# Optimization experiments

Measured on AMD Instinct MI355X. Metric: run time of the kernel, lower is better.

The kernel has to match this reference:

```python
import jax, jax.numpy as jnp
import numpy as np

INPUT_DIM, HID, LAT, FUT = 32, 128, 64, 128
B, T = 1024, 512


def _linear(x, W, b):
    return x @ W.T + b


def _lstm_layer(xs, Wih, Whh, b):
    # xs: [T, B, D_in] -> ys: [T, B, HID], h_T: [B, HID]
    Bsz = xs.shape[1]
    h0 = jnp.zeros((Bsz, HID), xs.dtype)
    c0 = jnp.zeros((Bsz, HID), xs.dtype)

    def step(carry, xt):
        h, c = carry
        g = xt @ Wih.T + h @ Whh.T + b  # [B, 4*HID]
        i, f, gg, o = jnp.split(g, 4, axis=-1)  # torch gate order i,f,g,o
        i = jax.nn.sigmoid(i)
        f = jax.nn.sigmoid(f)
        gg = jnp.tanh(gg)
        o = jax.nn.sigmoid(o)
        c = f * c + i * gg
        h = o * jnp.tanh(c)
        return (h, c), h

    (hT, _), ys = jax.lax.scan(step, (h0, c0), xs)
    return ys, hT


def setup_inputs() -> dict:
    key = jax.random.key(0)
    ks = iter(jax.random.split(key, 40))

    def w(shape, scale=0.05):
        return (jax.random.normal(next(ks), shape, dtype=jnp.float32) * scale)

    inp = {
        "x": jax.random.normal(next(ks), (B, T, INPUT_DIM), dtype=jnp.float32),
        "eps": jax.random.normal(next(ks), (B, LAT), dtype=jnp.float32),
        "u": jax.random.uniform(next(ks), (B, LAT), dtype=jnp.float32, minval=1e-4, maxval=1 - 1e-4),
        "choice": jax.random.uniform(next(ks), (B,), dtype=jnp.float32),
        # 3-layer LSTM params (torch: W_ih [4H, D], W_hh [4H, H], fused bias)
        "Wih0": w((4 * HID, INPUT_DIM)), "Whh0": w((4 * HID, HID)), "b0": w((4 * HID,)),
        "Wih1": w((4 * HID, HID)), "Whh1": w((4 * HID, HID)), "b1": w((4 * HID,)),
        "Wih2": w((4 * HID, HID)), "Whh2": w((4 * HID, HID)), "b2": w((4 * HID,)),
        "ln_g": jnp.ones((HID,), jnp.float32), "ln_b": jnp.zeros((HID,), jnp.float32),
        "fc1_W": w((128, HID)), "fc1_b": w((128,)),
        "fc2_W": w((64, 128)), "fc2_b": w((64,)),
        "mean_W": w((LAT, 64)), "mean_b": w((LAT,)),
        "logvar_W": w((LAT, 64)), "logvar_b": w((LAT,)),
        "scale_W": w((LAT, 64)), "scale_b": w((LAT,)),
        "shape_W": w((LAT, 64)), "shape_b": w((LAT,)),
        "dec1_W": w((128, LAT)), "dec1_b": w((128,)),
        "dec2_W": w((500, 128)), "dec2_b": w((500,)),
        "out_W": w((FUT, 500)), "out_b": w((FUT,)),
        "pi_params": jnp.array([3.0, 0.01], jnp.float32),
    }
    return inp


def reference(x, eps, u, choice,
              Wih0, Whh0, b0, Wih1, Whh1, b1, Wih2, Whh2, b2,
              ln_g, ln_b, fc1_W, fc1_b, fc2_W, fc2_b,
              mean_W, mean_b, logvar_W, logvar_b,
              scale_W, scale_b, shape_W, shape_b,
              dec1_W, dec1_b, dec2_W, dec2_b, out_W, out_b, pi_params):
    # --- Encoder ---
    xs = jnp.transpose(x, (1, 0, 2))  # [T, B, D]
    ys, _ = _lstm_layer(xs, Wih0, Whh0, b0)
    ys, _ = _lstm_layer(ys, Wih1, Whh1, b1)
    _, h = _lstm_layer(ys, Wih2, Whh2, b2)  # final hidden of last layer [B, HID]
    mu = h.mean(-1, keepdims=True)
    var = jnp.mean((h - mu) ** 2, -1, keepdims=True)
    h = (h - mu) * jax.lax.rsqrt(var + 1e-5) * ln_g + ln_b
    hid = jax.nn.relu(_linear(h, fc1_W, fc1_b))
    hid = jax.nn.relu(_linear(hid, fc2_W, fc2_b))  # dropout = identity (eval)
    z_mean = _linear(hid, mean_W, mean_b)
    z_logvar = _linear(hid, logvar_W, logvar_b)
    z_scale = jnp.exp(_linear(hid, scale_W, scale_b))
    z_shape = jnp.maximum(_linear(hid, shape_W, shape_b), 1e-6)
    # --- Reparameterize (vectorized mixture select) ---
    z_gauss = z_mean + eps * jnp.exp(0.5 * z_logvar)
    z_gpd = z_scale / z_shape * ((1.0 - u) ** (-z_shape) - 1.0)
    pi = jax.nn.softmax(pi_params)
    z = jnp.where((choice < pi[0])[:, None], z_gauss, z_gpd)
    # --- Decoder ---
    d = jax.nn.relu(_linear(z, dec1_W, dec1_b))
    d = jax.nn.relu(_linear(d, dec2_W, dec2_b))  # dropout = identity (eval)
    rec = _linear(d, out_W, out_b)
    return rec, z_mean, z_logvar, z_scale, z_shape
```

## Files before the change

### kernel.cpp

```cpp
#include <hip/hip_runtime.h>
#include <math.h>

typedef __attribute__((ext_vector_type(8))) short s16x8;
typedef __attribute__((ext_vector_type(4))) float f32x4;
typedef unsigned long long ull;

constexpr float LOG2E = 1.4426950408889634f;

__device__ __forceinline__ unsigned short f2bf(float f) {
  unsigned int x = __builtin_bit_cast(unsigned int, f);
  x += 0x7fffu + ((x >> 16) & 1u);
  return (unsigned short)(x >> 16);
}
__device__ __forceinline__ float fexp2(float x) { return __builtin_amdgcn_exp2f(x); }
__device__ __forceinline__ float frcp(float x)  { return __builtin_amdgcn_rcpf(x); }

#define MFMA16(A, B, Cc) __builtin_amdgcn_mfma_f32_16x16x32_bf16((A), (B), (Cc), 0, 0, 0)

constexpr int TT = 512;
constexpr int NB = 1024;
constexpr int CH = 2;

template <int DIN, bool FIRST, bool LAST>
__device__ __forceinline__ void scan_layer(
    unsigned short* x_s,
    unsigned short* h_s,
    float* b_s,
    const float* __restrict__ xin,
    unsigned short* ys,
    const float* __restrict__ Wih, const float* __restrict__ Whh,
    const float* __restrict__ bias, float* __restrict__ hT,
    int* prog_in, int* prog_out, int bblk)
{
  constexpr int KTX = DIN / 32;
  constexpr int XM  = (DIN == 32) ? 3 : 7;
  const int tid = threadIdx.x;
  const int wv = tid >> 6, ln = tid & 63, l15 = ln & 15, lg = ln >> 4;
  const int row0 = bblk * 16;
  const int prow = tid >> 5, pcol = tid & 31;

  s16x8 bfx[4][KTX], bfh[4][4];
#pragma unroll
  for (int j = 0; j < 4; ++j) {
    const float sc = (j == 2) ? (2.0f * LOG2E) : (-LOG2E);
    const int n = j * 128 + wv * 16 + l15;
#pragma unroll
    for (int kt = 0; kt < KTX; ++kt) {
      s16x8 f;
#pragma unroll
      for (int e = 0; e < 8; ++e) f[e] = (short)f2bf(Wih[n * DIN + kt * 32 + lg * 8 + e] * sc);
      bfx[j][kt] = f;
    }
#pragma unroll
    for (int kt = 0; kt < 4; ++kt) {
      s16x8 f;
#pragma unroll
      for (int e = 0; e < 8; ++e) f[e] = (short)f2bf(Whh[n * 128 + kt * 32 + lg * 8 + e] * sc);
      bfh[j][kt] = f;
    }
  }
  b_s[tid] = bias[tid] * ((tid >> 7) == 2 ? 2.0f * LOG2E : -LOG2E);
  for (int i = tid; i < 2 * 16 * 128; i += 512) h_s[i] = 0;

  float xrf[CH];
  ull xrh[CH];
  int avail = 0;
  if (FIRST) {
#pragma unroll
    for (int s = 0; s < CH; ++s) {
      xrf[s] = xin[(size_t)(row0 + prow) * (TT * 32) + s * 32 + pcol];
      x_s[s * (16 * DIN) + prow * DIN + (pcol ^ ((prow & XM) << 3))] = f2bf(xrf[s]);
    }
  } else {
    int f;
    do { f = __hip_atomic_load(prog_in, __ATOMIC_RELAXED, __HIP_MEMORY_SCOPE_AGENT); } while (f < 1);
    avail = f * CH;
#pragma unroll
    for (int s = 0; s < CH; ++s) {
      xrh[s] = __hip_atomic_load(
          (ull*)ys + ((size_t)s * (NB * 128) + (size_t)(row0 + prow) * 128 + pcol * 4) / 4,
          __ATOMIC_RELAXED, __HIP_MEMORY_SCOPE_AGENT);
      *reinterpret_cast<ull*>(
          &x_s[s * (16 * DIN) + prow * DIN + ((pcol * 4) ^ ((prow & 7) << 3))]) = xrh[s];
    }
  }
  __syncthreads();

  float cst[4] = {0.f, 0.f, 0.f, 0.f};
  const int hcol = wv * 16 + lg * 4;

  for (int t0 = 0; t0 < TT; t0 += CH) {
    const int t1 = t0 + CH;

    if (!LAST && tid == 0 && t0 > 0)
      __hip_atomic_store(prog_out, t0 / CH, __ATOMIC_RELAXED, __HIP_MEMORY_SCOPE_AGENT);

    int f_new = 0;
    if (!FIRST && t1 < TT)
      f_new = __hip_atomic_load(prog_in, __ATOMIC_RELAXED, __HIP_MEMORY_SCOPE_AGENT);

    bool prefetched = false;
    if (t1 < TT) {
      if (FIRST) {
#pragma unroll
        for (int s = 0; s < CH; ++s)
          xrf[s] = xin[(size_t)(row0 + prow) * (TT * 32) + (t1 + s) * 32 + pcol];
        prefetched = true;
      } else if (avail >= t1 + CH) {
#pragma unroll
        for (int s = 0; s < CH; ++s)
          xrh[s] = __hip_atomic_load(
              (ull*)ys + ((size_t)(t1 + s) * (NB * 128) + (size_t)(row0 + prow) * 128 + pcol * 4) / 4,
              __ATOMIC_RELAXED, __HIP_MEMORY_SCOPE_AGENT);
        prefetched = true;
      }
    }

    f32x4 gx[CH][4];
#pragma unroll
    for (int s = 0; s < CH; ++s) {
#pragma unroll
      for (int j = 0; j < 4; ++j)
        gx[s][j] = *reinterpret_cast<const f32x4*>(&b_s[j * 128 + wv * 16 + lg * 4]);
#pragma unroll
      for (int kt = 0; kt < KTX; ++kt) {
        const s16x8 xf = *reinterpret_cast<const s16x8*>(
            &x_s[s * (16 * DIN) + l15 * DIN + ((kt * 32 + lg * 8) ^ ((l15 & XM) << 3))]);
#pragma unroll
        for (int j = 0; j < 4; ++j) gx[s][j] = MFMA16(bfx[j][kt], xf, gx[s][j]);
      }
    }

    if (t1 < TT && !prefetched) {
      int f = f_new;
      while (f * CH < t1 + CH)
        f = __hip_atomic_load(prog_in, __ATOMIC_RELAXED, __HIP_MEMORY_SCOPE_AGENT);
      f_new = f;
      avail = f * CH;
#pragma unroll
      for (int s = 0; s < CH; ++s)
        xrh[s] = __hip_atomic_load(
            (ull*)ys + ((size_t)(t1 + s) * (NB * 128) + (size_t)(row0 + prow) * 128 + pcol * 4) / 4,
            __ATOMIC_RELAXED, __HIP_MEMORY_SCOPE_AGENT);
    }

#pragma unroll
    for (int s = 0; s < CH; ++s) {
      const int t = t0 + s;
      if (s) __syncthreads();
      unsigned short* buf  = h_s + (t & 1) * (16 * 128);
      unsigned short* nbuf = h_s + ((t + 1) & 1) * (16 * 128);
      s16x8 afr[4];
#pragma unroll
      for (int kt = 0; kt < 4; ++kt)
        afr[kt] = *reinterpret_cast<const s16x8*>(
            &buf[l15 * 128 + ((kt * 32 + lg * 8) ^ ((l15 & 7) << 3))]);
      f32x4 acc[4];
#pragma unroll
      for (int j = 0; j < 4; ++j) acc[j] = gx[s][j];
#pragma unroll
      for (int kt = 0; kt < 4; ++kt)
#pragma unroll
        for (int j = 0; j < 4; ++j) acc[j] = MFMA16(bfh[j][kt], afr[kt], acc[j]);

      float hv[4];
#pragma unroll
      for (int r = 0; r < 4; ++r) {
        const float iv = frcp(1.0f + fexp2(acc[0][r]));
        const float fv = frcp(1.0f + fexp2(acc[1][r]));
        const float gv = 1.0f - 2.0f * frcp(1.0f + fexp2(acc[2][r]));
        const float ov = frcp(1.0f + fexp2(acc[3][r]));
        const float cn = fv * cst[r] + iv * gv;
        cst[r] = cn;
        const float th = 1.0f - 2.0f * frcp(1.0f + fexp2(cn * (2.0f * LOG2E)));
        hv[r] = ov * th;
      }
      unsigned int plo, phi;
      asm("v_cvt_pk_bf16_f32 %0, %1, %2" : "=v"(plo) : "v"(hv[0]), "v"(hv[1]));
      asm("v_cvt_pk_bf16_f32 %0, %1, %2" : "=v"(phi) : "v"(hv[2]), "v"(hv[3]));
      const ull hpack = (ull)plo | ((ull)phi << 32);

      *reinterpret_cast<ull*>(&nbuf[l15 * 128 + (hcol ^ ((l15 & 7) << 3))]) = hpack;

      if (!LAST) {
        __hip_atomic_store(
            (ull*)ys + ((size_t)t * (NB * 128) + (size_t)(row0 + l15) * 128 + hcol) / 4,
            hpack, __ATOMIC_RELAXED, __HIP_MEMORY_SCOPE_AGENT);
      } else if (t == TT - 1) {
        f32x4 o = {hv[0], hv[1], hv[2], hv[3]};
        *reinterpret_cast<f32x4*>(&hT[(row0 + l15) * 128 + hcol]) = o;
      }

      if (s == CH - 1 && t1 < TT) {
        if (FIRST) {
#pragma unroll
          for (int ss = 0; ss < CH; ++ss)
            x_s[ss * (16 * DIN) + prow * DIN + (pcol ^ ((prow & XM) << 3))] = f2bf(xrf[ss]);
        } else {
#pragma unroll
          for (int ss = 0; ss < CH; ++ss)
            *reinterpret_cast<ull*>(
                &x_s[ss * (16 * DIN) + prow * DIN + ((pcol * 4) ^ ((prow & 7) << 3))]) = xrh[ss];
        }
      }
    }

    if (!FIRST && t1 < TT) {
      const int a2 = f_new * CH;
      if (a2 > avail) avail = a2;
    }

    __syncthreads();
  }

  if (!LAST && tid == 0)
    __hip_atomic_store(prog_out, TT / CH, __ATOMIC_RELAXED, __HIP_MEMORY_SCOPE_AGENT);
}

__global__ __launch_bounds__(512, 2) void lstm_fused(
    const float* __restrict__ x, unsigned short* ys,
    const float* __restrict__ Wih0, const float* __restrict__ Whh0, const float* __restrict__ b0,
    const float* __restrict__ Wih1, const float* __restrict__ Whh1, const float* __restrict__ b1,
    const float* __restrict__ Wih2, const float* __restrict__ Whh2, const float* __restrict__ b2,
    float* __restrict__ hT, int* prog)
{
  __shared__ unsigned short x_s[CH * 16 * 128];
  __shared__ unsigned short h_s[2 * 16 * 128];
  __shared__ float b_s[512];
  const int lay = blockIdx.x >> 6;
  const int bblk = blockIdx.x & 63;
  if (lay == 0) {
    scan_layer<32, true, false>(x_s, h_s, b_s, x, ys, Wih0, Whh0, b0, nullptr,
                                nullptr, &prog[(0 * 64 + bblk) * 16], bblk);
  } else if (lay == 1) {
    scan_layer<128, false, false>(x_s, h_s, b_s, nullptr, ys, Wih1, Whh1, b1, nullptr,
                                  &prog[(0 * 64 + bblk) * 16], &prog[(1 * 64 + bblk) * 16], bblk);
  } else {
    scan_layer<128, false, true>(x_s, h_s, b_s, nullptr, ys, Wih2, Whh2, b2, hT,
                                 &prog[(1 * 64 + bblk) * 16], nullptr, bblk);
  }
}

__global__ void init_flags(int* prog) {
  prog[threadIdx.x] = 0;
  prog[threadIdx.x + 1024] = 0;
}

__global__ __launch_bounds__(256) void head_kernel(
    const float* __restrict__ hT, const float* __restrict__ eps,
    const float* __restrict__ u, const float* __restrict__ choice,
    const float* __restrict__ ln_g, const float* __restrict__ ln_b,
    const float* __restrict__ fc1_W, const float* __restrict__ fc1_b,
    const float* __restrict__ fc2_W, const float* __restrict__ fc2_b,
    const float* __restrict__ mean_W, const float* __restrict__ mean_b,
    const float* __restrict__ logvar_W, const float* __restrict__ logvar_b,
    const float* __restrict__ scale_W, const float* __restrict__ scale_b,
    const float* __restrict__ shape_W, const float* __restrict__ shape_b,
    const float* __restrict__ dec1_W, const float* __restrict__ dec1_b,
    const float* __restrict__ dec2_W, const float* __restrict__ dec2_b,
    const float* __restrict__ out_W, const float* __restrict__ out_b,
    const float* __restrict__ pi_params, float* __restrict__ out)
{
  __shared__ float s_hn[4][128];
  __shared__ float s_a[4][128];
  __shared__ float s_b2[4][64];
  __shared__ float s_z[4][64];
  __shared__ float s_d1[4][128];
  __shared__ float s_d2[4][512];

  const int tid = threadIdx.x;
  const int gr0 = blockIdx.x * 4;

  {
    const int wvr = tid >> 6, lnn = tid & 63;
    const float v0 = hT[(gr0 + wvr) * 128 + lnn];
    const float v1 = hT[(gr0 + wvr) * 128 + 64 + lnn];
    float s = v0 + v1, s2 = v0 * v0 + v1 * v1;
#pragma unroll
    for (int off = 32; off; off >>= 1) {
      s  += __shfl_xor(s, off, 64);
      s2 += __shfl_xor(s2, off, 64);
    }
    const float mu  = s * (1.f / 128.f);
    const float var = s2 * (1.f / 128.f) - mu * mu;
    const float rs  = rsqrtf(var + 1e-5f);
    s_hn[wvr][lnn]      = (v0 - mu) * rs * ln_g[lnn]      + ln_b[lnn];
    s_hn[wvr][lnn + 64] = (v1 - mu) * rs * ln_g[lnn + 64] + ln_b[lnn + 64];
  }
  __syncthreads();
#pragma unroll
  for (int p = 0; p < 2; ++p) {
    const int idx = tid + p * 256, row = idx >> 7, col = idx & 127;
    const float* w = fc1_W + col * 128;
    float a = fc1_b[col];
    for (int k = 0; k < 128; k += 4)
      a += s_hn[row][k] * w[k] + s_hn[row][k + 1] * w[k + 1] +
           s_hn[row][k + 2] * w[k + 2] + s_hn[row][k + 3] * w[k + 3];
    s_a[row][col] = fmaxf(a, 0.f);
  }
  __syncthreads();
  {
    const int row = tid >> 6, col = tid & 63;
    const float* w = fc2_W + col * 128;
    float a = fc2_b[col];
    for (int k = 0; k < 128; ++k) a += s_a[row][k] * w[k];
    s_b2[row][col] = fmaxf(a, 0.f);
  }
  __syncthreads();
  {
    const int row = tid >> 6, c = tid & 63;
    const int gr = gr0 + row;
    float am = mean_b[c], al = logvar_b[c], as_ = scale_b[c], ah = shape_b[c];
    for (int k = 0; k < 64; ++k) {
      const float hv = s_b2[row][k];
      am  += hv * mean_W[c * 64 + k];
      al  += hv * logvar_W[c * 64 + k];
      as_ += hv * scale_W[c * 64 + k];
      ah  += hv * shape_W[c * 64 + k];
    }
    const float zsc = fexp2(as_ * LOG2E);
    const float zsh = fmaxf(ah, 1e-6f);
    out[131072 + gr * 64 + c] = am;
    out[196608 + gr * 64 + c] = al;
    out[262144 + gr * 64 + c] = zsc;
    out[327680 + gr * 64 + c] = zsh;
    const float ev = eps[gr * 64 + c], uv = u[gr * 64 + c], cv = choice[gr];
    const float zg = am + ev * fexp2(0.72134752044448170f * al);
    const float p0 = pi_params[0], p1 = pi_params[1];
    const float pi0 = 1.f / (1.f + expf(p1 - p0));
    const float tq = -zsh * logf(1.f - uv);
    const float zp = zsc * frcp(zsh) * expm1f(tq);
    s_z[row][c] = (cv < pi0) ? zg : zp;
  }
  __syncthreads();
#pragma unroll
  for (int p = 0; p < 2; ++p) {
    const int idx = tid + p * 256, row = idx >> 7, col = idx & 127;
    const float* w = dec1_W + col * 64;
    float a = dec1_b[col];
    for (int k = 0; k < 64; ++k) a += s_z[row][k] * w[k];
    s_d1[row][col] = fmaxf(a, 0.f);
  }
  __syncthreads();
  for (int o = tid; o < 2000; o += 256) {
    const int row = o / 500, col = o % 500;
    const float* w = dec2_W + col * 128;
    float a = dec2_b[col];
    for (int k = 0; k < 128; ++k) a += s_d1[row][k] * w[k];
    s_d2[row][col] = fmaxf(a, 0.f);
  }
  __syncthreads();
#pragma unroll
  for (int p = 0; p < 2; ++p) {
    const int idx = tid + p * 256, row = idx >> 7, col = idx & 127;
    const float* w = out_W + col * 500;
    float a = out_b[col];
    for (int k = 0; k < 500; ++k) a += s_d2[row][k] * w[k];
    out[(gr0 + row) * 128 + col] = a;
  }
}

extern "C" void kernel_launch(void* const* d_in, const int* in_sizes, int n_in,
                              void* d_out, int out_size, void* d_ws, size_t ws_size,
                              hipStream_t stream) {
  const float* x      = (const float*)d_in[0];
  const float* eps    = (const float*)d_in[1];
  const float* u      = (const float*)d_in[2];
  const float* choice = (const float*)d_in[3];
  const float* Wih0 = (const float*)d_in[4],  *Whh0 = (const float*)d_in[5],  *b0 = (const float*)d_in[6];
  const float* Wih1 = (const float*)d_in[7],  *Whh1 = (const float*)d_in[8],  *b1 = (const float*)d_in[9];
  const float* Wih2 = (const float*)d_in[10], *Whh2 = (const float*)d_in[11], *b2 = (const float*)d_in[12];
  const float* ln_g = (const float*)d_in[13], *ln_b = (const float*)d_in[14];
  const float* fc1_W = (const float*)d_in[15], *fc1_b = (const float*)d_in[16];
  const float* fc2_W = (const float*)d_in[17], *fc2_b = (const float*)d_in[18];
  const float* mean_W = (const float*)d_in[19], *mean_b = (const float*)d_in[20];
  const float* logvar_W = (const float*)d_in[21], *logvar_b = (const float*)d_in[22];
  const float* scale_W = (const float*)d_in[23], *scale_b = (const float*)d_in[24];
  const float* shape_W = (const float*)d_in[25], *shape_b = (const float*)d_in[26];
  const float* dec1_W = (const float*)d_in[27], *dec1_b = (const float*)d_in[28];
  const float* dec2_W = (const float*)d_in[29], *dec2_b = (const float*)d_in[30];
  const float* out_W = (const float*)d_in[31], *out_b = (const float*)d_in[32];
  const float* pi_params = (const float*)d_in[33];

  unsigned short* ys = (unsigned short*)d_ws;
  float* hT  = (float*)((char*)d_ws + (size_t)512 * 1024 * 128 * 2);
  int*   prog = (int*)((char*)d_ws + (size_t)512 * 1024 * 128 * 2 + (size_t)1024 * 128 * 4);

  init_flags<<<1, 1024, 0, stream>>>(prog);
  lstm_fused<<<192, 512, 0, stream>>>(x, ys, Wih0, Whh0, b0, Wih1, Whh1, b1,
                                      Wih2, Whh2, b2, hT, prog);
  head_kernel<<<256, 256, 0, stream>>>(hT, eps, u, choice, ln_g, ln_b,
      fc1_W, fc1_b, fc2_W, fc2_b, mean_W, mean_b, logvar_W, logvar_b,
      scale_W, scale_b, shape_W, shape_b, dec1_W, dec1_b, dec2_W, dec2_b,
      out_W, out_b, pi_params, (float*)d_out);
}
```

Baseline: 655.2 us.

## Process 32 batch rows per block and fuse LSTM gate math into one reciprocal

Each workgroup now handles two 16-row batch tiles (32 rows) instead of one, so the grid shrinks from 192 to 96 blocks and each block issues two independent MFMA chains per step. The recurrent weights held in registers are reused across both tiles, and the two chains give the scheduler interleaving. The gate nonlinearities are rewritten algebraically to share a few reciprocals, with clamped exponents to avoid overflow. Fewer blocks means less of the GPU is occupied, each block's serial per-step critical path grows, and the final progress store now waits on outstanding memory operations.

```diff
diff --git a/kernel.cpp b/kernel.cpp
--- a/kernel.cpp
+++ b/kernel.cpp
@@ -20,6 +20,20 @@
 constexpr int TT = 512;
 constexpr int NB = 1024;
 constexpr int CH = 2;
+
+__device__ __forceinline__ float lstm_cell(float ai, float af, float ag, float ao,
+                                           float& c) {
+  const float F = fexp2(fminf(af, 29.f));
+  const float I = fexp2(fminf(ai, 29.f));
+  const float G = fexp2(fminf(ag, 29.f));
+  const float O = fexp2(fminf(ao, 29.f));
+  const float P   = (1.f + I) * (1.f + G);
+  const float num = c * P + (G - 1.f) * (1.f + F);
+  const float cn  = num * frcp((1.f + F) * P);
+  c = cn;
+  const float E = fexp2(fminf(cn * (2.f * LOG2E), 60.f));
+  return (E - 1.f) * frcp((1.f + O) * (E + 1.f));
+}
 
 template <int DIN, bool FIRST, bool LAST>
 __device__ __forceinline__ void scan_layer(
@@ -36,57 +50,64 @@
   constexpr int XM  = (DIN == 32) ? 3 : 7;
   const int tid = threadIdx.x;
   const int wv = tid >> 6, ln = tid & 63, l15 = ln & 15, lg = ln >> 4;
-  const int row0 = bblk * 16;
-  const int prow = tid >> 5, pcol = tid & 31;
+  const int row0 = bblk * 32;
+  const int swzx = (l15 & XM) << 3;
+  const int swzh = (l15 & 7) << 3;
 
   s16x8 bfx[4][KTX], bfh[4][4];
 #pragma unroll
   for (int j = 0; j < 4; ++j) {
-    const float sc = (j == 2) ? (2.0f * LOG2E) : (-LOG2E);
+    const float scl = (j == 2) ? (2.0f * LOG2E) : (-LOG2E);
     const int n = j * 128 + wv * 16 + l15;
 #pragma unroll
     for (int kt = 0; kt < KTX; ++kt) {
       s16x8 f;
 #pragma unroll
-      for (int e = 0; e < 8; ++e) f[e] = (short)f2bf(Wih[n * DIN + kt * 32 + lg * 8 + e] * sc);
+      for (int e = 0; e < 8; ++e) f[e] = (short)f2bf(Wih[n * DIN + kt * 32 + lg * 8 + e] * scl);
       bfx[j][kt] = f;
     }
 #pragma unroll
     for (int kt = 0; kt < 4; ++kt) {
       s16x8 f;
 #pragma unroll
-      for (int e = 0; e < 8; ++e) f[e] = (short)f2bf(Whh[n * 128 + kt * 32 + lg * 8 + e] * sc);
+      for (int e = 0; e < 8; ++e) f[e] = (short)f2bf(Whh[n * 128 + kt * 32 + lg * 8 + e] * scl);
       bfh[j][kt] = f;
     }
   }
   b_s[tid] = bias[tid] * ((tid >> 7) == 2 ? 2.0f * LOG2E : -LOG2E);
-  for (int i = tid; i < 2 * 16 * 128; i += 512) h_s[i] = 0;
-
-  float xrf[CH];
-  ull xrh[CH];
+  for (int i = tid; i < 2 * 32 * 128; i += 512) h_s[i] = 0;
+
+  float xrf[CH][2];
+  ull   xrh[CH][2];
   int avail = 0;
   if (FIRST) {
 #pragma unroll
-    for (int s = 0; s < CH; ++s) {
-      xrf[s] = xin[(size_t)(row0 + prow) * (TT * 32) + s * 32 + pcol];
-      x_s[s * (16 * DIN) + prow * DIN + (pcol ^ ((prow & XM) << 3))] = f2bf(xrf[s]);
-    }
+    for (int s = 0; s < CH; ++s)
+#pragma unroll
+      for (int p = 0; p < 2; ++p) {
+        const int idx = p * 512 + tid, r = idx >> 5, c = idx & 31;
+        const float v = xin[(size_t)(row0 + r) * (TT * 32) + s * 32 + c];
+        x_s[s * (32 * 32) + r * 32 + (c ^ ((r & 3) << 3))] = f2bf(v);
+      }
   } else {
     int f;
     do { f = __hip_atomic_load(prog_in, __ATOMIC_RELAXED, __HIP_MEMORY_SCOPE_AGENT); } while (f < 1);
     avail = f * CH;
 #pragma unroll
-    for (int s = 0; s < CH; ++s) {
-      xrh[s] = __hip_atomic_load(
-          (ull*)ys + ((size_t)s * (NB * 128) + (size_t)(row0 + prow) * 128 + pcol * 4) / 4,
-          __ATOMIC_RELAXED, __HIP_MEMORY_SCOPE_AGENT);
-      *reinterpret_cast<ull*>(
-          &x_s[s * (16 * DIN) + prow * DIN + ((pcol * 4) ^ ((prow & 7) << 3))]) = xrh[s];
-    }
-  }
-  __syncthreads();
-
-  float cst[4] = {0.f, 0.f, 0.f, 0.f};
+    for (int s = 0; s < CH; ++s)
+#pragma unroll
+      for (int p = 0; p < 2; ++p) {
+        const int idx = p * 512 + tid, r = idx >> 5, ku = idx & 31;
+        const ull v = __hip_atomic_load(
+            (ull*)ys + ((size_t)s * (NB * 128) + (size_t)(row0 + r) * 128 + ku * 4) / 4,
+            __ATOMIC_RELAXED, __HIP_MEMORY_SCOPE_AGENT);
+        *reinterpret_cast<ull*>(&x_s[s * (32 * 128) + r * 128 + ((ku * 4) ^ ((r & 7) << 3))]) = v;
+      }
+  }
+  __syncthreads();
+
+  float cstA[4] = {0.f, 0.f, 0.f, 0.f};
+  float cstB[4] = {0.f, 0.f, 0.f, 0.f};
   const int hcol = wv * 16 + lg * 4;
 
   for (int t0 = 0; t0 < TT; t0 += CH) {
@@ -104,34 +125,49 @@
       if (FIRST) {
 #pragma unroll
         for (int s = 0; s < CH; ++s)
-          xrf[s] = xin[(size_t)(row0 + prow) * (TT * 32) + (t1 + s) * 32 + pcol];
+#pragma unroll
+          for (int p = 0; p < 2; ++p) {
+            const int idx = p * 512 + tid, r = idx >> 5, c = idx & 31;
+            xrf[s][p] = xin[(size_t)(row0 + r) * (TT * 32) + (t1 + s) * 32 + c];
+          }
         prefetched = true;
       } else if (avail >= t1 + CH) {
 #pragma unroll
         for (int s = 0; s < CH; ++s)
-          xrh[s] = __hip_atomic_load(
-              (ull*)ys + ((size_t)(t1 + s) * (NB * 128) + (size_t)(row0 + prow) * 128 + pcol * 4) / 4,
-              __ATOMIC_RELAXED, __HIP_MEMORY_SCOPE_AGENT);
+#pragma unroll
+          for (int p = 0; p < 2; ++p) {
+            const int idx = p * 512 + tid, r = idx >> 5, ku = idx & 31;
+            xrh[s][p] = __hip_atomic_load(
+                (ull*)ys + ((size_t)(t1 + s) * (NB * 128) + (size_t)(row0 + r) * 128 + ku * 4) / 4,
+                __ATOMIC_RELAXED, __HIP_MEMORY_SCOPE_AGENT);
+          }
         prefetched = true;
       }
     }
 
-    f32x4 gx[CH][4];
+    f32x4 gxA[CH][4], gxB[CH][4];
 #pragma unroll
     for (int s = 0; s < CH; ++s) {
 #pragma unroll
-      for (int j = 0; j < 4; ++j)
-        gx[s][j] = *reinterpret_cast<const f32x4*>(&b_s[j * 128 + wv * 16 + lg * 4]);
+      for (int j = 0; j < 4; ++j) {
+        const f32x4 bj = *reinterpret_cast<const f32x4*>(&b_s[j * 128 + wv * 16 + lg * 4]);
+        gxA[s][j] = bj; gxB[s][j] = bj;
+      }
 #pragma unroll
       for (int kt = 0; kt < KTX; ++kt) {
-        const s16x8 xf = *reinterpret_cast<const s16x8*>(
-            &x_s[s * (16 * DIN) + l15 * DIN + ((kt * 32 + lg * 8) ^ ((l15 & XM) << 3))]);
-#pragma unroll
-        for (int j = 0; j < 4; ++j) gx[s][j] = MFMA16(bfx[j][kt], xf, gx[s][j]);
-      }
-    }
-
-    if (t1 < TT && !prefetched) {
+        const s16x8 xfA = *reinterpret_cast<const s16x8*>(
+            &x_s[s * (32 * DIN) + l15 * DIN + ((kt * 32 + lg * 8) ^ swzx)]);
+        const s16x8 xfB = *reinterpret_cast<const s16x8*>(
+            &x_s[s * (32 * DIN) + (16 + l15) * DIN + ((kt * 32 + lg * 8) ^ swzx)]);
+#pragma unroll
+        for (int j = 0; j < 4; ++j) {
+          gxA[s][j] = MFMA16(bfx[j][kt], xfA, gxA[s][j]);
+          gxB[s][j] = MFMA16(bfx[j][kt], xfB, gxB[s][j]);
+        }
+      }
+    }
+
+    if (!FIRST && t1 < TT && !prefetched) {
       int f = f_new;
       while (f * CH < t1 + CH)
         f = __hip_atomic_load(prog_in, __ATOMIC_RELAXED, __HIP_MEMORY_SCOPE_AGENT);
@@ -139,82 +175,105 @@
       avail = f * CH;
 #pragma unroll
       for (int s = 0; s < CH; ++s)
-        xrh[s] = __hip_atomic_load(
-            (ull*)ys + ((size_t)(t1 + s) * (NB * 128) + (size_t)(row0 + prow) * 128 + pcol * 4) / 4,
-            __ATOMIC_RELAXED, __HIP_MEMORY_SCOPE_AGENT);
+#pragma unroll
+        for (int p = 0; p < 2; ++p) {
+          const int idx = p * 512 + tid, r = idx >> 5, ku = idx & 31;
+          xrh[s][p] = __hip_atomic_load(
+              (ull*)ys + ((size_t)(t1 + s) * (NB * 128) + (size_t)(row0 + r) * 128 + ku * 4) / 4,
+              __ATOMIC_RELAXED, __HIP_MEMORY_SCOPE_AGENT);
+        }
     }
 
 #pragma unroll
     for (int s = 0; s < CH; ++s) {
       const int t = t0 + s;
       if (s) __syncthreads();
-      unsigned short* buf  = h_s + (t & 1) * (16 * 128);
-      unsigned short* nbuf = h_s + ((t + 1) & 1) * (16 * 128);
-      s16x8 afr[4];
+      const unsigned short* buf = h_s + (t & 1) * (32 * 128);
+      unsigned short* nbuf = h_s + ((t + 1) & 1) * (32 * 128);
+
+      s16x8 afrA[4], afrB[4];
+#pragma unroll
+      for (int kt = 0; kt < 4; ++kt) {
+        afrA[kt] = *reinterpret_cast<const s16x8*>(
+            &buf[l15 * 128 + ((kt * 32 + lg * 8) ^ swzh)]);
+        afrB[kt] = *reinterpret_cast<const s16x8*>(
+            &buf[(16 + l15) * 128 + ((kt * 32 + lg * 8) ^ swzh)]);
+      }
+      f32x4 accA[4], accB[4];
+#pragma unroll
+      for (int j = 0; j < 4; ++j) { accA[j] = gxA[s][j]; accB[j] = gxB[s][j]; }
 #pragma unroll
       for (int kt = 0; kt < 4; ++kt)
-        afr[kt] = *reinterpret_cast<const s16x8*>(
-            &buf[l15 * 128 + ((kt * 32 + lg * 8) ^ ((l15 & 7) << 3))]);
-      f32x4 acc[4];
-#pragma unroll
-      for (int j = 0; j < 4; ++j) acc[j] = gx[s][j];
-#pragma unroll
-      for (int kt = 0; kt < 4; ++kt)
-#pragma unroll
-        for (int j = 0; j < 4; ++j) acc[j] = MFMA16(bfh[j][kt], afr[kt], acc[j]);
-
-      float hv[4];
+#pragma unroll
+        for (int j = 0; j < 4; ++j) {
+          accA[j] = MFMA16(bfh[j][kt], afrA[kt], accA[j]);
+          accB[j] = MFMA16(bfh[j][kt], afrB[kt], accB[j]);
+        }
+
+      float hvA[4], hvB[4];
 #pragma unroll
       for (int r = 0; r < 4; ++r) {
-        const float iv = frcp(1.0f + fexp2(acc[0][r]));
-        const float fv = frcp(1.0f + fexp2(acc[1][r]));
-        const float gv = 1.0f - 2.0f * frcp(1.0f + fexp2(acc[2][r]));
-        const float ov = frcp(1.0f + fexp2(acc[3][r]));
-        const float cn = fv * cst[r] + iv * gv;
-        cst[r] = cn;
-        const float th = 1.0f - 2.0f * frcp(1.0f + fexp2(cn * (2.0f * LOG2E)));
-        hv[r] = ov * th;
-      }
-      unsigned int plo, phi;
-      asm("v_cvt_pk_bf16_f32 %0, %1, %2" : "=v"(plo) : "v"(hv[0]), "v"(hv[1]));
-      asm("v_cvt_pk_bf16_f32 %0, %1, %2" : "=v"(phi) : "v"(hv[2]), "v"(hv[3]));
-      const ull hpack = (ull)plo | ((ull)phi << 32);
-
-      *reinterpret_cast<ull*>(&nbuf[l15 * 128 + (hcol ^ ((l15 & 7) << 3))]) = hpack;
+        hvA[r] = lstm_cell(accA[0][r], accA[1][r], accA[2][r], accA[3][r], cstA[r]);
+        hvB[r] = lstm_cell(accB[0][r], accB[1][r], accB[2][r], accB[3][r], cstB[r]);
+      }
+      unsigned int aLo, aHi, bLo, bHi;
+      asm("v_cvt_pk_bf16_f32 %0, %1, %2" : "=v"(aLo) : "v"(hvA[0]), "v"(hvA[1]));
+      asm("v_cvt_pk_bf16_f32 %0, %1, %2" : "=v"(aHi) : "v"(hvA[2]), "v"(hvA[3]));
+      asm("v_cvt_pk_bf16_f32 %0, %1, %2" : "=v"(bLo) : "v"(hvB[0]), "v"(hvB[1]));
+      asm("v_cvt_pk_bf16_f32 %0, %1, %2" : "=v"(bHi) : "v"(hvB[2]), "v"(hvB[3]));
+      const ull packA = (ull)aLo | ((ull)aHi << 32);
+      const ull packB = (ull)bLo | ((ull)bHi << 32);
+
+      *reinterpret_cast<ull*>(&nbuf[l15 * 128 + (hcol ^ swzh)]) = packA;
+      *reinterpret_cast<ull*>(&nbuf[(16 + l15) * 128 + (hcol ^ swzh)]) = packB;
 
       if (!LAST) {
         __hip_atomic_store(
             (ull*)ys + ((size_t)t * (NB * 128) + (size_t)(row0 + l15) * 128 + hcol) / 4,
-            hpack, __ATOMIC_RELAXED, __HIP_MEMORY_SCOPE_AGENT);
+            packA, __ATOMIC_RELAXED, __HIP_MEMORY_SCOPE_AGENT);
+        __hip_atomic_store(
+            (ull*)ys + ((size_t)t * (NB * 128) + (size_t)(row0 + 16 + l15) * 128 + hcol) / 4,
+            packB, __ATOMIC_RELAXED, __HIP_MEMORY_SCOPE_AGENT);
       } else if (t == TT - 1) {
-        f32x4 o = {hv[0], hv[1], hv[2], hv[3]};
-        *reinterpret_cast<f32x4*>(&hT[(row0 + l15) * 128 + hcol]) = o;
+        f32x4 oA = {hvA[0], hvA[1], hvA[2], hvA[3]};
+        f32x4 oB = {hvB[0], hvB[1], hvB[2], hvB[3]};
+        *reinterpret_cast<f32x4*>(&hT[(row0 + l15) * 128 + hcol]) = oA;
+        *reinterpret_cast<f32x4*>(&hT[(row0 + 16 + l15) * 128 + hcol]) = oB;
       }
 
       if (s == CH - 1 && t1 < TT) {
         if (FIRST) {
 #pragma unroll
           for (int ss = 0; ss < CH; ++ss)
-            x_s[ss * (16 * DIN) + prow * DIN + (pcol ^ ((prow & XM) << 3))] = f2bf(xrf[ss]);
+#pragma unroll
+            for (int p = 0; p < 2; ++p) {
+              const int idx = p * 512 + tid, r = idx >> 5, c = idx & 31;
+              x_s[ss * (32 * 32) + r * 32 + (c ^ ((r & 3) << 3))] = f2bf(xrf[ss][p]);
+            }
         } else {
 #pragma unroll
           for (int ss = 0; ss < CH; ++ss)
-            *reinterpret_cast<ull*>(
-                &x_s[ss * (16 * DIN) + prow * DIN + ((pcol * 4) ^ ((prow & 7) << 3))]) = xrh[ss];
+#pragma unroll
+            for (int p = 0; p < 2; ++p) {
+              const int idx = p * 512 + tid, r = idx >> 5, ku = idx & 31;
+              *reinterpret_cast<ull*>(
+                  &x_s[ss * (32 * 128) + r * 128 + ((ku * 4) ^ ((r & 7) << 3))]) = xrh[ss][p];
+            }
         }
       }
     }
 
-    if (!FIRST && t1 < TT) {
-      const int a2 = f_new * CH;
-      if (a2 > avail) avail = a2;
-    }
+    if (!FIRST && f_new * CH > avail) avail = f_new * CH;
 
     __syncthreads();
   }
 
-  if (!LAST && tid == 0)
-    __hip_atomic_store(prog_out, TT / CH, __ATOMIC_RELAXED, __HIP_MEMORY_SCOPE_AGENT);
+  if (!LAST) {
+    asm volatile("s_waitcnt vmcnt(0)" ::: "memory");
+    __syncthreads();
+    if (tid == 0)
+      __hip_atomic_store(prog_out, TT / CH, __ATOMIC_RELAXED, __HIP_MEMORY_SCOPE_AGENT);
+  }
 }
 
 __global__ __launch_bounds__(512, 2) void lstm_fused(
@@ -224,20 +283,20 @@
     const float* __restrict__ Wih2, const float* __restrict__ Whh2, const float* __restrict__ b2,
     float* __restrict__ hT, int* prog)
 {
-  __shared__ unsigned short x_s[CH * 16 * 128];
-  __shared__ unsigned short h_s[2 * 16 * 128];
+  __shared__ unsigned short x_s[CH * 32 * 128];
+  __shared__ unsigned short h_s[2 * 32 * 128];
   __shared__ float b_s[512];
-  const int lay = blockIdx.x >> 6;
-  const int bblk = blockIdx.x & 63;
+  const int lay = blockIdx.x >> 5;
+  const int bblk = blockIdx.x & 31;
   if (lay == 0) {
     scan_layer<32, true, false>(x_s, h_s, b_s, x, ys, Wih0, Whh0, b0, nullptr,
-                                nullptr, &prog[(0 * 64 + bblk) * 16], bblk);
+                                nullptr, &prog[bblk * 16], bblk);
   } else if (lay == 1) {
     scan_layer<128, false, false>(x_s, h_s, b_s, nullptr, ys, Wih1, Whh1, b1, nullptr,
-                                  &prog[(0 * 64 + bblk) * 16], &prog[(1 * 64 + bblk) * 16], bblk);
+                                  &prog[bblk * 16], &prog[(32 + bblk) * 16], bblk);
   } else {
     scan_layer<128, false, true>(x_s, h_s, b_s, nullptr, ys, Wih2, Whh2, b2, hT,
-                                 &prog[(1 * 64 + bblk) * 16], nullptr, bblk);
+                                 &prog[(32 + bblk) * 16], nullptr, bblk);
   }
 }
 
@@ -387,8 +446,8 @@
   int*   prog = (int*)((char*)d_ws + (size_t)512 * 1024 * 128 * 2 + (size_t)1024 * 128 * 4);
 
   init_flags<<<1, 1024, 0, stream>>>(prog);
-  lstm_fused<<<192, 512, 0, stream>>>(x, ys, Wih0, Whh0, b0, Wih1, Whh1, b1,
-                                      Wih2, Whh2, b2, hT, prog);
+  lstm_fused<<<96, 512, 0, stream>>>(x, ys, Wih0, Whh0, b0, Wih1, Whh1, b1,
+                                     Wih2, Whh2, b2, hT, prog);
   head_kernel<<<256, 256, 0, stream>>>(hT, eps, u, choice, ln_g, ln_b,
       fc1_W, fc1_b, fc2_W, fc2_b, mean_W, mean_b, logvar_W, logvar_b,
       scale_W, scale_b, shape_W, shape_b, dec1_W, dec1_b, dec2_W, dec2_b,
```

New measurement: 1.156 ms. +76.4%, slower.
